# Performance work log

Measured on AMD Instinct MI355X. Metric: run time of the kernel, lower is better.

## Reference

```python
import jax, jax.numpy as jnp
import numpy as np

NUM_SEGMENTS = 64  # batch_size, = batch_indices.max()+1 by construction


def setup_inputs() -> dict:
    key = jax.random.key(0)
    k1, k2 = jax.random.split(key)
    N, D = 1048576, 256
    features = jax.random.normal(k1, (N, D), dtype=jnp.float32)
    batch_indices = jnp.sort(jax.random.randint(k2, (N,), 0, NUM_SEGMENTS, dtype=jnp.int64))
    return {"features": features, "batch_indices": batch_indices}


def reference(features, batch_indices):
    # features: [N, D], batch_indices: [N] -> out: [B, 2*D]
    idx = batch_indices.astype(jnp.int32)
    counts = jax.ops.segment_sum(jnp.ones_like(features[:, 0]), idx,
                                 num_segments=NUM_SEGMENTS)  # [B]
    sums = jax.ops.segment_sum(features, idx, num_segments=NUM_SEGMENTS)  # [B, D]
    nonempty = counts > 0
    mean_feat = sums / jnp.maximum(counts, 1.0)[:, None]
    maxs = jax.ops.segment_max(features, idx, num_segments=NUM_SEGMENTS)  # [B, D]
    max_feat = jnp.where(nonempty[:, None], maxs, 0.0)
    mean_feat = jnp.where(nonempty[:, None], mean_feat, 0.0)
    return jnp.concatenate([mean_feat, max_feat], axis=1)  # [B, 2*D]
```

## Files before the change

kernel.cpp:

```cpp
#include <hip/hip_runtime.h>
#include <math.h>

#define D 256
#define SEGS 64
#define RPB 512
#define THREADS 256

__device__ __forceinline__ unsigned enc_f32(float f) {
  unsigned u = __float_as_uint(f);
  return (u & 0x80000000u) ? ~u : (u | 0x80000000u);
}
__device__ __forceinline__ float dec_f32(unsigned k) {
  unsigned u = (k & 0x80000000u) ? (k ^ 0x80000000u) : ~k;
  return __uint_as_float(u);
}

__global__ void detect_kernel(const int* __restrict__ idx, int n, int* flag) {
  if (blockIdx.x == 0 && threadIdx.x == 0)
    *flag = (idx[(size_t)n - 1] == 0) ? 2 : 1;
}

__global__ void hist_kernel(const int* __restrict__ idx, int n,
                            const int* __restrict__ flag,
                            int* __restrict__ counts) {
  __shared__ int h[SEGS];
  if (threadIdx.x < SEGS) h[threadIdx.x] = 0;
  __syncthreads();
  const int stride = *flag;
  int gid = blockIdx.x * blockDim.x + threadIdx.x;
  int gsz = gridDim.x * blockDim.x;
  for (int i = gid; i < n; i += gsz) {
    int s = idx[(size_t)i * stride];
    atomicAdd(&h[s & (SEGS - 1)], 1);
  }
  __syncthreads();
  if (threadIdx.x < SEGS) atomicAdd(&counts[threadIdx.x], h[threadIdx.x]);
}

__global__ __launch_bounds__(THREADS, 8)
void agg_kernel(const float* __restrict__ feat, const int* __restrict__ idx,
                const int* __restrict__ flag, float* __restrict__ sums,
                unsigned* __restrict__ maxk, int n) {
  __shared__ int s_idx[RPB];
  const int stride = *flag;
  const int r0 = blockIdx.x * RPB;
  const int rows = min(RPB, n - r0);

  for (int i = threadIdx.x; i < rows; i += THREADS)
    s_idx[i] = idx[(size_t)(r0 + i) * stride];
  __syncthreads();

  const int lane = threadIdx.x & 63;
  const int wave = threadIdx.x >> 6;
  const int rb = wave * (RPB / 4);
  const int re = min(rb + (RPB / 4), rows);
  if (rb >= rows) return;

  float4 sum = make_float4(0.f, 0.f, 0.f, 0.f);
  float4 mx  = make_float4(-INFINITY, -INFINITY, -INFINITY, -INFINITY);
  int cur = s_idx[rb];

  const float* base = feat + (size_t)r0 * D + lane * 4;

  for (int i = rb; i < re; ++i) {
    int s = s_idx[i];
    if (s != cur) {
      float* sp = sums + cur * D + lane * 4;
      atomicAdd(sp + 0, sum.x); atomicAdd(sp + 1, sum.y);
      atomicAdd(sp + 2, sum.z); atomicAdd(sp + 3, sum.w);
      unsigned* mp = maxk + cur * D + lane * 4;
      atomicMax(mp + 0, enc_f32(mx.x)); atomicMax(mp + 1, enc_f32(mx.y));
      atomicMax(mp + 2, enc_f32(mx.z)); atomicMax(mp + 3, enc_f32(mx.w));
      sum = make_float4(0.f, 0.f, 0.f, 0.f);
      mx  = make_float4(-INFINITY, -INFINITY, -INFINITY, -INFINITY);
      cur = s;
    }
    const float4 v = *reinterpret_cast<const float4*>(base + (size_t)i * D);
    sum.x += v.x; sum.y += v.y; sum.z += v.z; sum.w += v.w;
    mx.x = fmaxf(mx.x, v.x); mx.y = fmaxf(mx.y, v.y);
    mx.z = fmaxf(mx.z, v.z); mx.w = fmaxf(mx.w, v.w);
  }

  float* sp = sums + cur * D + lane * 4;
  atomicAdd(sp + 0, sum.x); atomicAdd(sp + 1, sum.y);
  atomicAdd(sp + 2, sum.z); atomicAdd(sp + 3, sum.w);
  unsigned* mp = maxk + cur * D + lane * 4;
  atomicMax(mp + 0, enc_f32(mx.x)); atomicMax(mp + 1, enc_f32(mx.y));
  atomicMax(mp + 2, enc_f32(mx.z)); atomicMax(mp + 3, enc_f32(mx.w));
}

__global__ void finalize_kernel(const float* __restrict__ sums,
                                const unsigned* __restrict__ maxk,
                                const int* __restrict__ counts,
                                float* __restrict__ out) {
  int i = blockIdx.x * blockDim.x + threadIdx.x;
  if (i >= SEGS * 2 * D) return;
  int s = i / (2 * D);
  int j = i % (2 * D);
  int c = counts[s];
  float v;
  if (j < D)
    v = (c > 0) ? sums[s * D + j] / (float)c : 0.0f;
  else
    v = (c > 0) ? dec_f32(maxk[s * D + (j - D)]) : 0.0f;
  out[i] = v;
}

extern "C" void kernel_launch(void* const* d_in, const int* in_sizes, int n_in,
                              void* d_out, int out_size, void* d_ws, size_t ws_size,
                              hipStream_t stream) {
  const float* feat = (const float*)d_in[0];
  const int*   idx  = (const int*)d_in[1];
  const int n = in_sizes[1];
  float* out = (float*)d_out;

  char* ws = (char*)d_ws;
  float*    sums   = (float*)ws;
  unsigned* maxk   = (unsigned*)(ws + SEGS * D * 4);
  int*      counts = (int*)(ws + 2 * SEGS * D * 4);
  int*      flag   = counts + SEGS;

  const size_t zero_bytes = 2 * (size_t)SEGS * D * 4 + SEGS * 4;
  hipMemsetAsync(ws, 0, zero_bytes, stream);

  detect_kernel<<<1, 64, 0, stream>>>(idx, n, flag);
  hist_kernel<<<512, 256, 0, stream>>>(idx, n, flag, counts);

  const int nblocks = (n + RPB - 1) / RPB;
  agg_kernel<<<nblocks, THREADS, 0, stream>>>(feat, idx, flag, sums, maxk, n);

  finalize_kernel<<<(SEGS * 2 * D + 255) / 256, 256, 0, stream>>>(
      sums, maxk, counts, out);
}
```

Measured before the change: 258.9 us.

## Fold segment counting into aggregation kernel and run-length inner loop

Removes the separate detect and histogram kernels. The aggregation kernel now computes the index stride inline and accumulates per-segment counts from run lengths using one atomic per wave-run. The inner loop is restructured to find each run boundary first and then stream rows branch-free with nontemporal vector loads and unrolling. This saves two launches and a full pass over the index array, at the cost of every block re-reading the last index element.

```diff
diff --git a/kernel.cpp b/kernel.cpp
--- a/kernel.cpp
+++ b/kernel.cpp
@@ -5,6 +5,8 @@
 #define SEGS 64
 #define RPB 512
 #define THREADS 256
+
+typedef float f32x4 __attribute__((ext_vector_type(4)));
 
 __device__ __forceinline__ unsigned enc_f32(float f) {
   unsigned u = __float_as_uint(f);
@@ -15,34 +17,16 @@
   return __uint_as_float(u);
 }
 
-__global__ void detect_kernel(const int* __restrict__ idx, int n, int* flag) {
-  if (blockIdx.x == 0 && threadIdx.x == 0)
-    *flag = (idx[(size_t)n - 1] == 0) ? 2 : 1;
-}
-
-__global__ void hist_kernel(const int* __restrict__ idx, int n,
-                            const int* __restrict__ flag,
-                            int* __restrict__ counts) {
-  __shared__ int h[SEGS];
-  if (threadIdx.x < SEGS) h[threadIdx.x] = 0;
-  __syncthreads();
-  const int stride = *flag;
-  int gid = blockIdx.x * blockDim.x + threadIdx.x;
-  int gsz = gridDim.x * blockDim.x;
-  for (int i = gid; i < n; i += gsz) {
-    int s = idx[(size_t)i * stride];
-    atomicAdd(&h[s & (SEGS - 1)], 1);
-  }
-  __syncthreads();
-  if (threadIdx.x < SEGS) atomicAdd(&counts[threadIdx.x], h[threadIdx.x]);
+__device__ __forceinline__ int idx_stride(const int* idx, int n) {
+  return (idx[(size_t)n - 1] == 0) ? 2 : 1;
 }
 
 __global__ __launch_bounds__(THREADS, 8)
 void agg_kernel(const float* __restrict__ feat, const int* __restrict__ idx,
-                const int* __restrict__ flag, float* __restrict__ sums,
-                unsigned* __restrict__ maxk, int n) {
+                float* __restrict__ sums, unsigned* __restrict__ maxk,
+                int* __restrict__ counts, int n) {
   __shared__ int s_idx[RPB];
-  const int stride = *flag;
+  const int stride = idx_stride(idx, n);
   const int r0 = blockIdx.x * RPB;
   const int rows = min(RPB, n - r0);
 
@@ -52,41 +36,46 @@
 
   const int lane = threadIdx.x & 63;
   const int wave = threadIdx.x >> 6;
-  const int rb = wave * (RPB / 4);
-  const int re = min(rb + (RPB / 4), rows);
-  if (rb >= rows) return;
-
-  float4 sum = make_float4(0.f, 0.f, 0.f, 0.f);
-  float4 mx  = make_float4(-INFINITY, -INFINITY, -INFINITY, -INFINITY);
-  int cur = s_idx[rb];
+  int i = wave * (RPB / 4);
+  const int re = min(i + (RPB / 4), rows);
+  if (i >= re) return;
 
   const float* base = feat + (size_t)r0 * D + lane * 4;
+  const int last = s_idx[re - 1];
 
-  for (int i = rb; i < re; ++i) {
-    int s = s_idx[i];
-    if (s != cur) {
-      float* sp = sums + cur * D + lane * 4;
-      atomicAdd(sp + 0, sum.x); atomicAdd(sp + 1, sum.y);
-      atomicAdd(sp + 2, sum.z); atomicAdd(sp + 3, sum.w);
-      unsigned* mp = maxk + cur * D + lane * 4;
-      atomicMax(mp + 0, enc_f32(mx.x)); atomicMax(mp + 1, enc_f32(mx.y));
-      atomicMax(mp + 2, enc_f32(mx.z)); atomicMax(mp + 3, enc_f32(mx.w));
-      sum = make_float4(0.f, 0.f, 0.f, 0.f);
-      mx  = make_float4(-INFINITY, -INFINITY, -INFINITY, -INFINITY);
-      cur = s;
+  while (i < re) {
+    const int cur = s_idx[i];
+    int j;
+    if (cur == last) {
+      j = re;
+    } else {
+      j = i + 1;
+      while (s_idx[j] == cur) ++j;
     }
-    const float4 v = *reinterpret_cast<const float4*>(base + (size_t)i * D);
-    sum.x += v.x; sum.y += v.y; sum.z += v.z; sum.w += v.w;
-    mx.x = fmaxf(mx.x, v.x); mx.y = fmaxf(mx.y, v.y);
-    mx.z = fmaxf(mx.z, v.z); mx.w = fmaxf(mx.w, v.w);
+
+    f32x4 sum = {0.f, 0.f, 0.f, 0.f};
+    f32x4 mx  = {-INFINITY, -INFINITY, -INFINITY, -INFINITY};
+#pragma unroll 4
+    for (int k = i; k < j; ++k) {
+      const f32x4 v = __builtin_nontemporal_load(
+          reinterpret_cast<const f32x4*>(base + (size_t)k * D));
+      sum += v;
+      mx.x = __builtin_fmaxf(mx.x, v.x);
+      mx.y = __builtin_fmaxf(mx.y, v.y);
+      mx.z = __builtin_fmaxf(mx.z, v.z);
+      mx.w = __builtin_fmaxf(mx.w, v.w);
+    }
+
+    float* sp = sums + cur * D + lane * 4;
+    atomicAdd(sp + 0, sum.x); atomicAdd(sp + 1, sum.y);
+    atomicAdd(sp + 2, sum.z); atomicAdd(sp + 3, sum.w);
+    unsigned* mp = maxk + cur * D + lane * 4;
+    atomicMax(mp + 0, enc_f32(mx.x)); atomicMax(mp + 1, enc_f32(mx.y));
+    atomicMax(mp + 2, enc_f32(mx.z)); atomicMax(mp + 3, enc_f32(mx.w));
+    if (lane == 0) atomicAdd(&counts[cur], j - i);
+
+    i = j;
   }
-
-  float* sp = sums + cur * D + lane * 4;
-  atomicAdd(sp + 0, sum.x); atomicAdd(sp + 1, sum.y);
-  atomicAdd(sp + 2, sum.z); atomicAdd(sp + 3, sum.w);
-  unsigned* mp = maxk + cur * D + lane * 4;
-  atomicMax(mp + 0, enc_f32(mx.x)); atomicMax(mp + 1, enc_f32(mx.y));
-  atomicMax(mp + 2, enc_f32(mx.z)); atomicMax(mp + 3, enc_f32(mx.w));
 }
 
 __global__ void finalize_kernel(const float* __restrict__ sums,
@@ -118,16 +107,12 @@
   float*    sums   = (float*)ws;
   unsigned* maxk   = (unsigned*)(ws + SEGS * D * 4);
   int*      counts = (int*)(ws + 2 * SEGS * D * 4);
-  int*      flag   = counts + SEGS;
 
   const size_t zero_bytes = 2 * (size_t)SEGS * D * 4 + SEGS * 4;
   hipMemsetAsync(ws, 0, zero_bytes, stream);
 
-  detect_kernel<<<1, 64, 0, stream>>>(idx, n, flag);
-  hist_kernel<<<512, 256, 0, stream>>>(idx, n, flag, counts);
-
   const int nblocks = (n + RPB - 1) / RPB;
-  agg_kernel<<<nblocks, THREADS, 0, stream>>>(feat, idx, flag, sums, maxk, n);
+  agg_kernel<<<nblocks, THREADS, 0, stream>>>(feat, idx, sums, maxk, counts, n);
 
   finalize_kernel<<<(SEGS * 2 * D + 255) / 256, 256, 0, stream>>>(
       sums, maxk, counts, out);
```

Result: faster. 217.8 us (-15.9%).
